# Kernel optimization log

Hardware: AMD Instinct MI355X
Metric: run time of the kernel (lower is better)

The kernel has to match this reference:

```python
import jax, jax.numpy as jnp
import numpy as np

NUM_MODES = 256
THRESHOLD = 1.0
ATAN_ALPHA = 2.0

@jax.custom_vjp
def atan_spike(u):
    # snntorch ATan surrogate: forward heaviside(u > 0)
    return (u > 0).astype(u.dtype)

def _atan_fwd(u):
    return atan_spike(u), u

def _atan_bwd(u, g):
    # grad = alpha/2 / (1 + (pi/2 * alpha * u)^2)
    return (g * (ATAN_ALPHA / 2.0) / (1.0 + (jnp.pi / 2.0 * ATAN_ALPHA * u) ** 2),)

atan_spike.defvjp(_atan_fwd, _atan_bwd)

def setup_inputs() -> dict:
    key = jax.random.key(0)
    k0, k1, k2, k3, k4 = jax.random.split(key, 5)
    B, N, P = 8192, 256, 32
    x = jax.random.normal(k0, (B, N), dtype=jnp.float32)
    W_lin = jax.random.normal(k1, (N, N), dtype=jnp.float32) * 0.05
    b_lin = jax.random.normal(k2, (N,), dtype=jnp.float32) * 0.05
    W_sel = jax.random.normal(k3, (P, NUM_MODES, N), dtype=jnp.float32) * 0.05
    b_sel = jax.random.normal(k4, (P, NUM_MODES), dtype=jnp.float32) * 0.05
    return {"x": x, "W_lin": W_lin, "b_lin": b_lin, "W_sel": W_sel, "b_sel": b_sel}

def reference(x, W_lin, b_lin, W_sel, b_sel):
    B = x.shape[0]
    # lin
    h = x @ W_lin.T + b_lin                       # [B, N]
    # regular Leaky, single step, mem=None: mem = beta*0 + h = h
    reg_mem = h
    reg_out = atan_spike(reg_mem - THRESHOLD)      # [B, N]
    # polymorphic neurons (vectorized over P):
    # mode selector scores: softmax over modes
    scores = jax.nn.softmax(jnp.einsum('bn,pmn->bpm', reg_out, W_sel) + b_sel, axis=-1)  # [B,P,M]
    # all NUM_MODES Leaky modes see mem=None -> mem = reg_out, identical spikes
    spk_mode = atan_spike(reg_out - THRESHOLD)     # [B, N] (N == NUM_MODES)
    # mixed = sum_i spk_i * scores = NUM_MODES * spk * scores (broadcast over mode/neuron axis)
    mixed = NUM_MODES * spk_mode[:, None, :] * scores  # [B, P, N]
    out = jnp.concatenate([reg_out, mixed.reshape(B, -1)], axis=-1)  # [B, N*(1+P)]
    return out
```

## Files before the change

### kernel.cpp

```cpp
#include <hip/hip_runtime.h>
#include <hip/hip_bf16.h>


#define SNN_B 8192
#define SNN_N 256
#define SNN_P 32
#define SNN_ROW (SNN_N * (SNN_P + 1))
#define BLK_ROWS 16

__global__ __launch_bounds__(256) void w_transpose_kernel(
    const float* __restrict__ W, float* __restrict__ WT)
{
    const int o = blockIdx.x * 256 + threadIdx.x;
    const int k = o >> 8, n = o & 255;
    WT[o] = W[n * SNN_N + k];
}

__global__ __launch_bounds__(256) void polysnn_main_kernel(
    const float* __restrict__ x,
    const float* __restrict__ W,
    const float* __restrict__ WT,
    const float* __restrict__ bias,
    float* __restrict__ out)
{
    __shared__ float xs[BLK_ROWS][SNN_N];

    const int tid  = threadIdx.x;
    const int lane = tid & 63;
    const int wave = tid >> 6;
    const int row0 = blockIdx.x * BLK_ROWS;

    {
        const float4* x4  = reinterpret_cast<const float4*>(x + (size_t)row0 * SNN_N);
        float4*       xs4 = reinterpret_cast<float4*>(&xs[0][0]);
#pragma unroll
        for (int i = 0; i < 4; ++i) xs4[tid + i * 256] = x4[tid + i * 256];
    }
    __syncthreads();

    const int grow0 = row0 + wave * 4;
    const float4* wt4 = reinterpret_cast<const float4*>(WT);
    const float4* xs4 = reinterpret_cast<const float4*>(&xs[0][0]);
    const int xbase = wave * 4 * 64;

    float acc[4][4];
#pragma unroll
    for (int r = 0; r < 4; ++r)
#pragma unroll
        for (int c = 0; c < 4; ++c) acc[r][c] = 0.0f;

    float4 wcur0 = wt4[0 * 64 + lane];
    float4 wcur1 = wt4[1 * 64 + lane];
    float4 wcur2 = wt4[2 * 64 + lane];
    float4 wcur3 = wt4[3 * 64 + lane];
    float4 xcur[4];
#pragma unroll
    for (int r = 0; r < 4; ++r) xcur[r] = xs4[xbase + r * 64 + 0];

    float* const wfill = out + (size_t)grow0 * SNN_ROW;
    const float4 z = make_float4(0.f, 0.f, 0.f, 0.f);

    for (int i = 0; i < 64; ++i) {
        const int ip = (i + 1) & 63;
        float4 wnx0 = wt4[(ip * 4 + 0) * 64 + lane];
        float4 wnx1 = wt4[(ip * 4 + 1) * 64 + lane];
        float4 wnx2 = wt4[(ip * 4 + 2) * 64 + lane];
        float4 wnx3 = wt4[(ip * 4 + 3) * 64 + lane];
        float4 xnxt[4];
#pragma unroll
        for (int r = 0; r < 4; ++r) xnxt[r] = xs4[xbase + r * 64 + ip];

#pragma unroll
        for (int j = 0; j < 2; ++j) {
            const int fidx = ((i * 2 + j) << 6) + lane;
            const int rl   = fidx >> 11;
            const int c4   = fidx & 2047;
            *reinterpret_cast<float4*>(wfill + rl * SNN_ROW + SNN_N + (c4 << 2)) = z;
        }

#pragma unroll
        for (int r = 0; r < 4; ++r) {
            const float4 xr = xcur[r];
            acc[r][0] = fmaf(xr.x, wcur0.x, acc[r][0]);
            acc[r][1] = fmaf(xr.x, wcur0.y, acc[r][1]);
            acc[r][2] = fmaf(xr.x, wcur0.z, acc[r][2]);
            acc[r][3] = fmaf(xr.x, wcur0.w, acc[r][3]);
            acc[r][0] = fmaf(xr.y, wcur1.x, acc[r][0]);
            acc[r][1] = fmaf(xr.y, wcur1.y, acc[r][1]);
            acc[r][2] = fmaf(xr.y, wcur1.z, acc[r][2]);
            acc[r][3] = fmaf(xr.y, wcur1.w, acc[r][3]);
            acc[r][0] = fmaf(xr.z, wcur2.x, acc[r][0]);
            acc[r][1] = fmaf(xr.z, wcur2.y, acc[r][1]);
            acc[r][2] = fmaf(xr.z, wcur2.z, acc[r][2]);
            acc[r][3] = fmaf(xr.z, wcur2.w, acc[r][3]);
            acc[r][0] = fmaf(xr.w, wcur3.x, acc[r][0]);
            acc[r][1] = fmaf(xr.w, wcur3.y, acc[r][1]);
            acc[r][2] = fmaf(xr.w, wcur3.z, acc[r][2]);
            acc[r][3] = fmaf(xr.w, wcur3.w, acc[r][3]);
        }

        wcur0 = wnx0; wcur1 = wnx1; wcur2 = wnx2; wcur3 = wnx3;
#pragma unroll
        for (int r = 0; r < 4; ++r) xcur[r] = xnxt[r];
    }

    const float4 bb = reinterpret_cast<const float4*>(bias)[lane];
#pragma unroll
    for (int r = 0; r < 4; ++r) {
        float h[4] = {acc[r][0] + bb.x, acc[r][1] + bb.y,
                      acc[r][2] + bb.z, acc[r][3] + bb.w};
        float s[4];
#pragma unroll
        for (int c = 0; c < 4; ++c) {
            if (__builtin_expect(fabsf(h[c] - 1.0f) < 1e-3f, 0)) {
                const int n = 4 * lane + c;
                double a = (double)bias[n];
                const float* wr = W + (size_t)n * SNN_N;
                for (int k = 0; k < SNN_N; ++k)
                    a += (double)wr[k] * (double)xs[wave * 4 + r][k];
                s[c] = (a > 1.0) ? 1.0f : 0.0f;
            } else {
                s[c] = (h[c] > 1.0f) ? 1.0f : 0.0f;
            }
        }
        *reinterpret_cast<float4*>(out + (size_t)(grow0 + r) * SNN_ROW + (lane << 2))
            = make_float4(s[0], s[1], s[2], s[3]);
    }
}

__global__ __launch_bounds__(256) void polysnn_mono_kernel(
    const float* __restrict__ x, const float* __restrict__ W,
    const float* __restrict__ bias, float* __restrict__ out)
{
    __shared__ float xs[8][SNN_N];
    const int tid = threadIdx.x;
    const int row0 = blockIdx.x * 8;
    {
        const float4* x4  = reinterpret_cast<const float4*>(x + (size_t)row0 * SNN_N);
        float4*       xs4 = reinterpret_cast<float4*>(&xs[0][0]);
        xs4[tid] = x4[tid]; xs4[tid + 256] = x4[tid + 256];
    }
    __syncthreads();
    const float4 zz = make_float4(0.f, 0.f, 0.f, 0.f);
#pragma unroll
    for (int r = 0; r < 8; ++r) {
        float4* o4 = reinterpret_cast<float4*>(out + (size_t)(row0 + r) * SNN_ROW + SNN_N);
#pragma unroll
        for (int i = 0; i < 8; ++i) o4[tid + i * 256] = zz;
    }
    const int n = tid;
    float acc[8];
#pragma unroll
    for (int r = 0; r < 8; ++r) acc[r] = 0.0f;
    const float4* w4  = reinterpret_cast<const float4*>(W + (size_t)n * SNN_N);
    const float4* xs4 = reinterpret_cast<const float4*>(&xs[0][0]);
#pragma unroll 4
    for (int k4 = 0; k4 < SNN_N / 4; ++k4) {
        const float4 w = w4[k4];
#pragma unroll
        for (int r = 0; r < 8; ++r) {
            const float4 xr = xs4[r * 64 + k4];
            acc[r] = fmaf(w.x, xr.x, acc[r]); acc[r] = fmaf(w.y, xr.y, acc[r]);
            acc[r] = fmaf(w.z, xr.z, acc[r]); acc[r] = fmaf(w.w, xr.w, acc[r]);
        }
    }
    const float bn = bias[n];
#pragma unroll
    for (int r = 0; r < 8; ++r) {
        const float h = acc[r] + bn;
        float spike;
        if (__builtin_expect(fabsf(h - 1.0f) < 1e-3f, 0)) {
            double a = (double)bn;
            const float* wr = W + (size_t)n * SNN_N;
            for (int k = 0; k < SNN_N; ++k) a += (double)wr[k] * (double)xs[r][k];
            spike = (a > 1.0) ? 1.0f : 0.0f;
        } else spike = (h > 1.0f) ? 1.0f : 0.0f;
        out[(size_t)(row0 + r) * SNN_ROW + n] = spike;
    }
}

extern "C" void kernel_launch(void* const* d_in, const int* in_sizes, int n_in,
                              void* d_out, int out_size, void* d_ws, size_t ws_size,
                              hipStream_t stream) {
    const float* x     = (const float*)d_in[0];
    const float* W_lin = (const float*)d_in[1];
    const float* b_lin = (const float*)d_in[2];
    float* out = (float*)d_out;

    if (ws_size >= (size_t)SNN_N * SNN_N * sizeof(float)) {
        float* WT = (float*)d_ws;
        w_transpose_kernel<<<256, 256, 0, stream>>>(W_lin, WT);
        polysnn_main_kernel<<<SNN_B / BLK_ROWS, 256, 0, stream>>>(x, W_lin, WT, b_lin, out);
    } else {
        polysnn_mono_kernel<<<SNN_B / 8, 256, 0, stream>>>(x, W_lin, b_lin, out);
    }
}
```

Measured before the change: 59.86 us.

## Halve rows per block and deepen weight prefetch to two stages

```diff
diff --git a/kernel.cpp b/kernel.cpp
--- a/kernel.cpp
+++ b/kernel.cpp
@@ -6,7 +6,7 @@
 #define SNN_N 256
 #define SNN_P 32
 #define SNN_ROW (SNN_N * (SNN_P + 1))
-#define BLK_ROWS 16
+#define BLK_ROWS 8
 
 __global__ __launch_bounds__(256) void w_transpose_kernel(
     const float* __restrict__ W, float* __restrict__ WT)
@@ -16,7 +16,7 @@
     WT[o] = W[n * SNN_N + k];
 }
 
-__global__ __launch_bounds__(256) void polysnn_main_kernel(
+__global__ __launch_bounds__(256, 4) void polysnn_main_kernel(
     const float* __restrict__ x,
     const float* __restrict__ W,
     const float* __restrict__ WT,
@@ -32,81 +32,112 @@
 
     {
         const float4* x4  = reinterpret_cast<const float4*>(x + (size_t)row0 * SNN_N);
-        float4*       xs4 = reinterpret_cast<float4*>(&xs[0][0]);
-#pragma unroll
-        for (int i = 0; i < 4; ++i) xs4[tid + i * 256] = x4[tid + i * 256];
+        float4*       xsw = reinterpret_cast<float4*>(&xs[0][0]);
+        xsw[tid]       = x4[tid];
+        xsw[tid + 256] = x4[tid + 256];
     }
     __syncthreads();
 
-    const int grow0 = row0 + wave * 4;
+    const int grow0 = row0 + wave * 2;
     const float4* wt4 = reinterpret_cast<const float4*>(WT);
     const float4* xs4 = reinterpret_cast<const float4*>(&xs[0][0]);
-    const int xbase = wave * 4 * 64;
-
-    float acc[4][4];
-#pragma unroll
-    for (int r = 0; r < 4; ++r)
+    const int xbase = wave * 2 * 64;
+
+    float acc[2][4];
+#pragma unroll
+    for (int r = 0; r < 2; ++r)
 #pragma unroll
         for (int c = 0; c < 4; ++c) acc[r][c] = 0.0f;
 
-    float4 wcur0 = wt4[0 * 64 + lane];
-    float4 wcur1 = wt4[1 * 64 + lane];
-    float4 wcur2 = wt4[2 * 64 + lane];
-    float4 wcur3 = wt4[3 * 64 + lane];
-    float4 xcur[4];
-#pragma unroll
-    for (int r = 0; r < 4; ++r) xcur[r] = xs4[xbase + r * 64 + 0];
+    float4 wa0 = wt4[(0 * 4 + 0) * 64 + lane];
+    float4 wa1 = wt4[(0 * 4 + 1) * 64 + lane];
+    float4 wa2 = wt4[(0 * 4 + 2) * 64 + lane];
+    float4 wa3 = wt4[(0 * 4 + 3) * 64 + lane];
+    float4 wb0 = wt4[(1 * 4 + 0) * 64 + lane];
+    float4 wb1 = wt4[(1 * 4 + 1) * 64 + lane];
+    float4 wb2 = wt4[(1 * 4 + 2) * 64 + lane];
+    float4 wb3 = wt4[(1 * 4 + 3) * 64 + lane];
+    float4 xc0 = xs4[xbase + 0 * 64 + 0];
+    float4 xc1 = xs4[xbase + 1 * 64 + 0];
 
     float* const wfill = out + (size_t)grow0 * SNN_ROW;
     const float4 z = make_float4(0.f, 0.f, 0.f, 0.f);
 
-    for (int i = 0; i < 64; ++i) {
-        const int ip = (i + 1) & 63;
-        float4 wnx0 = wt4[(ip * 4 + 0) * 64 + lane];
-        float4 wnx1 = wt4[(ip * 4 + 1) * 64 + lane];
-        float4 wnx2 = wt4[(ip * 4 + 2) * 64 + lane];
-        float4 wnx3 = wt4[(ip * 4 + 3) * 64 + lane];
-        float4 xnxt[4];
-#pragma unroll
-        for (int r = 0; r < 4; ++r) xnxt[r] = xs4[xbase + r * 64 + ip];
-
-#pragma unroll
-        for (int j = 0; j < 2; ++j) {
-            const int fidx = ((i * 2 + j) << 6) + lane;
-            const int rl   = fidx >> 11;
-            const int c4   = fidx & 2047;
-            *reinterpret_cast<float4*>(wfill + rl * SNN_ROW + SNN_N + (c4 << 2)) = z;
-        }
-
-#pragma unroll
-        for (int r = 0; r < 4; ++r) {
-            const float4 xr = xcur[r];
-            acc[r][0] = fmaf(xr.x, wcur0.x, acc[r][0]);
-            acc[r][1] = fmaf(xr.x, wcur0.y, acc[r][1]);
-            acc[r][2] = fmaf(xr.x, wcur0.z, acc[r][2]);
-            acc[r][3] = fmaf(xr.x, wcur0.w, acc[r][3]);
-            acc[r][0] = fmaf(xr.y, wcur1.x, acc[r][0]);
-            acc[r][1] = fmaf(xr.y, wcur1.y, acc[r][1]);
-            acc[r][2] = fmaf(xr.y, wcur1.z, acc[r][2]);
-            acc[r][3] = fmaf(xr.y, wcur1.w, acc[r][3]);
-            acc[r][0] = fmaf(xr.z, wcur2.x, acc[r][0]);
-            acc[r][1] = fmaf(xr.z, wcur2.y, acc[r][1]);
-            acc[r][2] = fmaf(xr.z, wcur2.z, acc[r][2]);
-            acc[r][3] = fmaf(xr.z, wcur2.w, acc[r][3]);
-            acc[r][0] = fmaf(xr.w, wcur3.x, acc[r][0]);
-            acc[r][1] = fmaf(xr.w, wcur3.y, acc[r][1]);
-            acc[r][2] = fmaf(xr.w, wcur3.z, acc[r][2]);
-            acc[r][3] = fmaf(xr.w, wcur3.w, acc[r][3]);
-        }
-
-        wcur0 = wnx0; wcur1 = wnx1; wcur2 = wnx2; wcur3 = wnx3;
-#pragma unroll
-        for (int r = 0; r < 4; ++r) xcur[r] = xnxt[r];
-    }
+#define SNN_FMA_BLOCK(W0, W1, W2, W3)                                   \
+    do {                                                                \
+        acc[0][0] = fmaf(xc0.x, W0.x, acc[0][0]);                       \
+        acc[0][1] = fmaf(xc0.x, W0.y, acc[0][1]);                       \
+        acc[0][2] = fmaf(xc0.x, W0.z, acc[0][2]);                       \
+        acc[0][3] = fmaf(xc0.x, W0.w, acc[0][3]);                       \
+        acc[0][0] = fmaf(xc0.y, W1.x, acc[0][0]);                       \
+        acc[0][1] = fmaf(xc0.y, W1.y, acc[0][1]);                       \
+        acc[0][2] = fmaf(xc0.y, W1.z, acc[0][2]);                       \
+        acc[0][3] = fmaf(xc0.y, W1.w, acc[0][3]);                       \
+        acc[0][0] = fmaf(xc0.z, W2.x, acc[0][0]);                       \
+        acc[0][1] = fmaf(xc0.z, W2.y, acc[0][1]);                       \
+        acc[0][2] = fmaf(xc0.z, W2.z, acc[0][2]);                       \
+        acc[0][3] = fmaf(xc0.z, W2.w, acc[0][3]);                       \
+        acc[0][0] = fmaf(xc0.w, W3.x, acc[0][0]);                       \
+        acc[0][1] = fmaf(xc0.w, W3.y, acc[0][1]);                       \
+        acc[0][2] = fmaf(xc0.w, W3.z, acc[0][2]);                       \
+        acc[0][3] = fmaf(xc0.w, W3.w, acc[0][3]);                       \
+        acc[1][0] = fmaf(xc1.x, W0.x, acc[1][0]);                       \
+        acc[1][1] = fmaf(xc1.x, W0.y, acc[1][1]);                       \
+        acc[1][2] = fmaf(xc1.x, W0.z, acc[1][2]);                       \
+        acc[1][3] = fmaf(xc1.x, W0.w, acc[1][3]);                       \
+        acc[1][0] = fmaf(xc1.y, W1.x, acc[1][0]);                       \
+        acc[1][1] = fmaf(xc1.y, W1.y, acc[1][1]);                       \
+        acc[1][2] = fmaf(xc1.y, W1.z, acc[1][2]);                       \
+        acc[1][3] = fmaf(xc1.y, W1.w, acc[1][3]);                       \
+        acc[1][0] = fmaf(xc1.z, W2.x, acc[1][0]);                       \
+        acc[1][1] = fmaf(xc1.z, W2.y, acc[1][1]);                       \
+        acc[1][2] = fmaf(xc1.z, W2.z, acc[1][2]);                       \
+        acc[1][3] = fmaf(xc1.z, W2.w, acc[1][3]);                       \
+        acc[1][0] = fmaf(xc1.w, W3.x, acc[1][0]);                       \
+        acc[1][1] = fmaf(xc1.w, W3.y, acc[1][1]);                       \
+        acc[1][2] = fmaf(xc1.w, W3.z, acc[1][2]);                       \
+        acc[1][3] = fmaf(xc1.w, W3.w, acc[1][3]);                       \
+    } while (0)
+
+    for (int i = 0; i < 64; i += 2) {
+        {
+            const int ip = (i + 2) & 63;
+            float4 t0 = wt4[(ip * 4 + 0) * 64 + lane];
+            float4 t1 = wt4[(ip * 4 + 1) * 64 + lane];
+            float4 t2 = wt4[(ip * 4 + 2) * 64 + lane];
+            float4 t3 = wt4[(ip * 4 + 3) * 64 + lane];
+            const int ixp = (i + 1) & 63;
+            float4 xn0 = xs4[xbase + 0 * 64 + ixp];
+            float4 xn1 = xs4[xbase + 1 * 64 + ixp];
+            const int fidx = (i << 6) + lane;
+            *reinterpret_cast<float4*>(
+                wfill + (fidx >> 11) * SNN_ROW + SNN_N + ((fidx & 2047) << 2)) = z;
+            SNN_FMA_BLOCK(wa0, wa1, wa2, wa3);
+            wa0 = t0; wa1 = t1; wa2 = t2; wa3 = t3;
+            xc0 = xn0; xc1 = xn1;
+        }
+        {
+            const int ip = (i + 3) & 63;
+            float4 t0 = wt4[(ip * 4 + 0) * 64 + lane];
+            float4 t1 = wt4[(ip * 4 + 1) * 64 + lane];
+            float4 t2 = wt4[(ip * 4 + 2) * 64 + lane];
+            float4 t3 = wt4[(ip * 4 + 3) * 64 + lane];
+            const int ixp = (i + 2) & 63;
+            float4 xn0 = xs4[xbase + 0 * 64 + ixp];
+            float4 xn1 = xs4[xbase + 1 * 64 + ixp];
+            const int fidx = ((i + 1) << 6) + lane;
+            *reinterpret_cast<float4*>(
+                wfill + (fidx >> 11) * SNN_ROW + SNN_N + ((fidx & 2047) << 2)) = z;
+            SNN_FMA_BLOCK(wb0, wb1, wb2, wb3);
+            wb0 = t0; wb1 = t1; wb2 = t2; wb3 = t3;
+            xc0 = xn0; xc1 = xn1;
+        }
+    }
+#undef SNN_FMA_BLOCK
 
     const float4 bb = reinterpret_cast<const float4*>(bias)[lane];
 #pragma unroll
-    for (int r = 0; r < 4; ++r) {
+    for (int r = 0; r < 2; ++r) {
         float h[4] = {acc[r][0] + bb.x, acc[r][1] + bb.y,
                       acc[r][2] + bb.z, acc[r][3] + bb.w};
         float s[4];
@@ -117,7 +148,7 @@
                 double a = (double)bias[n];
                 const float* wr = W + (size_t)n * SNN_N;
                 for (int k = 0; k < SNN_N; ++k)
-                    a += (double)wr[k] * (double)xs[wave * 4 + r][k];
+                    a += (double)wr[k] * (double)xs[wave * 2 + r][k];
                 s[c] = (a > 1.0) ? 1.0f : 0.0f;
             } else {
                 s[c] = (h[c] > 1.0f) ? 1.0f : 0.0f;
@@ -137,8 +168,8 @@
     const int row0 = blockIdx.x * 8;
     {
         const float4* x4  = reinterpret_cast<const float4*>(x + (size_t)row0 * SNN_N);
-        float4*       xs4 = reinterpret_cast<float4*>(&xs[0][0]);
-        xs4[tid] = x4[tid]; xs4[tid + 256] = x4[tid + 256];
+        float4*       xsw = reinterpret_cast<float4*>(&xs[0][0]);
+        xsw[tid] = x4[tid]; xsw[tid + 256] = x4[tid + 256];
     }
     __syncthreads();
     const float4 zz = make_float4(0.f, 0.f, 0.f, 0.f);
```

Result: slower. 67.15 us (+12.2%).
